# Kernel optimization log

Measured on AMD Instinct MI355X. Metric: run time of the kernel, lower is better.

## Reference

```python
import jax, jax.numpy as jnp
import numpy as np

INPUT_SIZE = 64
STATE_SIZE = 1984
OUTPUT_SIZE = 64
WIDTH = INPUT_SIZE + STATE_SIZE  # 2048
ID_PROP = 0.9
SEQ_LEN = 128
BATCH = 128


def setup_inputs() -> dict:
    key = jax.random.key(0)
    k1, k2, k3 = jax.random.split(key, 3)
    # xavier-uniform bound for square [WIDTH, WIDTH] linears
    bound = float(np.sqrt(6.0 / (WIDTH + WIDTH)))
    W1 = jax.random.uniform(k1, (WIDTH, WIDTH), jnp.float32, -bound, bound)
    W2 = jax.random.uniform(k2, (WIDTH, WIDTH), jnp.float32, -bound, bound)
    b1 = jnp.zeros((WIDTH,), jnp.float32)
    b2 = jnp.zeros((WIDTH,), jnp.float32)
    inp = jax.random.normal(k3, (SEQ_LEN, BATCH, INPUT_SIZE), jnp.float32)
    return {"input": inp, "W1": W1, "b1": b1, "W2": W2, "b2": b2}


def reference(input, W1, b1, W2, b2):
    T, B, _ = input.shape
    # initial output_stream is zeros of width WIDTH, broadcast over batch
    state0 = jnp.zeros((B, WIDTH), input.dtype)

    def step(state, x_t):
        # Shift: concat(input, state) then keep first WIDTH elems
        s = jnp.concatenate([x_t, state[:, :STATE_SIZE]], axis=-1)  # [B, WIDTH]
        # Res: r*p + (1-p) * fc2(|fc1(s)|)
        h = jnp.abs(s @ W1.T + b1)
        s = s * ID_PROP + (1.0 - ID_PROP) * (h @ W2.T + b2)
        return s, None

    state, _ = jax.lax.scan(step, state0, input)
    return state[..., -OUTPUT_SIZE:]
```

## Files before the change

### kernel.cpp

```cpp
#include <hip/hip_runtime.h>
#include <stdint.h>


#define NSTEPS 128
#define NB 128
#define WID 2048
#define SS 1984

typedef __attribute__((ext_vector_type(8))) short short8;
typedef __attribute__((ext_vector_type(4))) short short4v;
typedef __attribute__((ext_vector_type(4))) float f32x4;
typedef unsigned long long u64;

static __device__ __forceinline__ short f2bf(float f) {
  union { float f; unsigned u; } v; v.f = f;
  unsigned r = (v.u + 0x7fffu + ((v.u >> 16) & 1u)) >> 16;
  return (short)r;
}

static __device__ __forceinline__ short8 pack8(f32x4 lo, f32x4 hi) {
  short8 r;
  r[0] = f2bf(lo[0]); r[1] = f2bf(lo[1]); r[2] = f2bf(lo[2]); r[3] = f2bf(lo[3]);
  r[4] = f2bf(hi[0]); r[5] = f2bf(hi[1]); r[6] = f2bf(hi[2]); r[7] = f2bf(hi[3]);
  return r;
}

static __device__ __forceinline__ void ast64(void* p, u64 v) {
  __hip_atomic_store((u64*)p, v, __ATOMIC_RELAXED, __HIP_MEMORY_SCOPE_AGENT);
}
static __device__ __forceinline__ unsigned ald32(const unsigned* p) {
  return __hip_atomic_load(p, __ATOMIC_RELAXED, __HIP_MEMORY_SCOPE_AGENT);
}

#define LLCLD(d, a) \
  asm volatile("global_load_dwordx4 %0, %1, off sc1" : "=&v"(d) : "v"(a))
#define VMW(n) do { \
    asm volatile("s_waitcnt vmcnt(" #n ")" ::: "memory"); \
    __builtin_amdgcn_sched_barrier(0); \
  } while (0)

#define P1ISSUE(b, X) do {                                                    \
    if (kb == 0 && (b) == 0) {   \
      const float* q0_ = inp + ((size_t)t * NB + m0) * 64 + q8;               \
      const float* q1_ = inp + ((size_t)t * NB + m1) * 64 + q8;               \
      X[0] = pack8(*(const f32x4*)q0_, *(const f32x4*)(q0_ + 4));             \
      X[1] = pack8(*(const f32x4*)q1_, *(const f32x4*)(q1_ + 4));             \
      X[2] = pack8(*(const f32x4*)(q0_ + 32), *(const f32x4*)(q0_ + 36));     \
      X[3] = pack8(*(const f32x4*)(q1_ + 32), *(const f32x4*)(q1_ + 36));     \
      const short* s_ = SbOld + (size_t)slabL * 1024;                         \
      LLCLD(X[4], (s_ + rowoff0));           LLCLD(X[5], (s_ + rowoff1));     \
      LLCLD(X[6], (s_ + 4096 + rowoff0));    LLCLD(X[7], (s_ + 4096 + rowoff1)); \
    } else {                                                                  \
      const short* s_ = SbOld + (size_t)(kb / 8 + 16 * (b) - 8 + slabL) * 1024; \
      LLCLD(X[0], (s_ + rowoff0));           LLCLD(X[1], (s_ + rowoff1));     \
      LLCLD(X[2], (s_ + 4096 + rowoff0));    LLCLD(X[3], (s_ + 4096 + rowoff1)); \
      LLCLD(X[4], (s_ + 8192 + rowoff0));    LLCLD(X[5], (s_ + 8192 + rowoff1)); \
      LLCLD(X[6], (s_ + 12288 + rowoff0));   LLCLD(X[7], (s_ + 12288 + rowoff1)); \
    }                                                                         \
  } while (0)

#define P1MFMA(b, X) do {                                                     \
    a00 = __builtin_amdgcn_mfma_f32_16x16x32_bf16(X[0], B1[4*(b)+0][0], a00, 0,0,0); \
    a01 = __builtin_amdgcn_mfma_f32_16x16x32_bf16(X[0], B1[4*(b)+0][1], a01, 0,0,0); \
    a10 = __builtin_amdgcn_mfma_f32_16x16x32_bf16(X[1], B1[4*(b)+0][0], a10, 0,0,0); \
    a11 = __builtin_amdgcn_mfma_f32_16x16x32_bf16(X[1], B1[4*(b)+0][1], a11, 0,0,0); \
    a00 = __builtin_amdgcn_mfma_f32_16x16x32_bf16(X[2], B1[4*(b)+1][0], a00, 0,0,0); \
    a01 = __builtin_amdgcn_mfma_f32_16x16x32_bf16(X[2], B1[4*(b)+1][1], a01, 0,0,0); \
    a10 = __builtin_amdgcn_mfma_f32_16x16x32_bf16(X[3], B1[4*(b)+1][0], a10, 0,0,0); \
    a11 = __builtin_amdgcn_mfma_f32_16x16x32_bf16(X[3], B1[4*(b)+1][1], a11, 0,0,0); \
    a00 = __builtin_amdgcn_mfma_f32_16x16x32_bf16(X[4], B1[4*(b)+2][0], a00, 0,0,0); \
    a01 = __builtin_amdgcn_mfma_f32_16x16x32_bf16(X[4], B1[4*(b)+2][1], a01, 0,0,0); \
    a10 = __builtin_amdgcn_mfma_f32_16x16x32_bf16(X[5], B1[4*(b)+2][0], a10, 0,0,0); \
    a11 = __builtin_amdgcn_mfma_f32_16x16x32_bf16(X[5], B1[4*(b)+2][1], a11, 0,0,0); \
    a00 = __builtin_amdgcn_mfma_f32_16x16x32_bf16(X[6], B1[4*(b)+3][0], a00, 0,0,0); \
    a01 = __builtin_amdgcn_mfma_f32_16x16x32_bf16(X[6], B1[4*(b)+3][1], a01, 0,0,0); \
    a10 = __builtin_amdgcn_mfma_f32_16x16x32_bf16(X[7], B1[4*(b)+3][0], a10, 0,0,0); \
    a11 = __builtin_amdgcn_mfma_f32_16x16x32_bf16(X[7], B1[4*(b)+3][1], a11, 0,0,0); \
  } while (0)

#define P2ISSUE(b, X) do {                                                    \
    const short* h_ = hb + (size_t)(kb / 8 + 16 * (b) + slabL) * 1024;        \
    LLCLD(X[0], (h_ + rowoff0));           LLCLD(X[1], (h_ + rowoff1));       \
    LLCLD(X[2], (h_ + 4096 + rowoff0));    LLCLD(X[3], (h_ + 4096 + rowoff1)); \
    LLCLD(X[4], (h_ + 8192 + rowoff0));    LLCLD(X[5], (h_ + 8192 + rowoff1)); \
    LLCLD(X[6], (h_ + 12288 + rowoff0));   LLCLD(X[7], (h_ + 12288 + rowoff1)); \
  } while (0)

#define P2MFMA(b, X) do {                                                     \
    c00 = __builtin_amdgcn_mfma_f32_16x16x32_bf16(X[0], B2[4*(b)+0][0], c00, 0,0,0); \
    c01 = __builtin_amdgcn_mfma_f32_16x16x32_bf16(X[0], B2[4*(b)+0][1], c01, 0,0,0); \
    c10 = __builtin_amdgcn_mfma_f32_16x16x32_bf16(X[1], B2[4*(b)+0][0], c10, 0,0,0); \
    c11 = __builtin_amdgcn_mfma_f32_16x16x32_bf16(X[1], B2[4*(b)+0][1], c11, 0,0,0); \
    c00 = __builtin_amdgcn_mfma_f32_16x16x32_bf16(X[2], B2[4*(b)+1][0], c00, 0,0,0); \
    c01 = __builtin_amdgcn_mfma_f32_16x16x32_bf16(X[2], B2[4*(b)+1][1], c01, 0,0,0); \
    c10 = __builtin_amdgcn_mfma_f32_16x16x32_bf16(X[3], B2[4*(b)+1][0], c10, 0,0,0); \
    c11 = __builtin_amdgcn_mfma_f32_16x16x32_bf16(X[3], B2[4*(b)+1][1], c11, 0,0,0); \
    c00 = __builtin_amdgcn_mfma_f32_16x16x32_bf16(X[4], B2[4*(b)+2][0], c00, 0,0,0); \
    c01 = __builtin_amdgcn_mfma_f32_16x16x32_bf16(X[4], B2[4*(b)+2][1], c01, 0,0,0); \
    c10 = __builtin_amdgcn_mfma_f32_16x16x32_bf16(X[5], B2[4*(b)+2][0], c10, 0,0,0); \
    c11 = __builtin_amdgcn_mfma_f32_16x16x32_bf16(X[5], B2[4*(b)+2][1], c11, 0,0,0); \
    c00 = __builtin_amdgcn_mfma_f32_16x16x32_bf16(X[6], B2[4*(b)+3][0], c00, 0,0,0); \
    c01 = __builtin_amdgcn_mfma_f32_16x16x32_bf16(X[6], B2[4*(b)+3][1], c01, 0,0,0); \
    c10 = __builtin_amdgcn_mfma_f32_16x16x32_bf16(X[7], B2[4*(b)+3][0], c10, 0,0,0); \
    c11 = __builtin_amdgcn_mfma_f32_16x16x32_bf16(X[7], B2[4*(b)+3][1], c11, 0,0,0); \
  } while (0)

__global__ __launch_bounds__(256, 1)
void resrnn_kernel(const float* __restrict__ inp, const float* __restrict__ W1,
                   const float* __restrict__ b1f, const float* __restrict__ W2,
                   const float* __restrict__ b2f, float* __restrict__ out,
                   unsigned char* __restrict__ ws)
{
  const int tid   = threadIdx.x;
  const int bid   = blockIdx.x;
  const int group = bid & 3;
  const int chunk = bid >> 2;
  const int mbase = group * 32;
  const int n0    = chunk * 32;
  const int wave  = tid >> 6;
  const int lane  = tid & 63;
  const int l15   = lane & 15;
  const int q8    = (lane >> 4) * 8;
  const int kb    = wave * 512;
  const int slabL = lane >> 4;

  unsigned* sgen = (unsigned*)(ws + group * 8192);
  unsigned* hgen = (unsigned*)(ws + group * 8192 + 4096);
  float* Sf0 = (float*)(ws + 32768);
  float* Sf1 = (float*)(ws + 32768 + 1015808);
  short* Sb0 = (short*)(ws + 32768 + 2031616);
  short* Sb1 = (short*)(ws + 32768 + 2539520);
  short* hb  = (short*)(ws + 32768 + 3047424);

  __shared__ float red[4][16][65];

  short8 B1[16][2], B2[16][2];
#pragma unroll
  for (int ks = 0; ks < 16; ++ks) {
#pragma unroll
    for (int nt = 0; nt < 2; ++nt) {
      const float* p1 = W1 + (size_t)(n0 + nt * 16 + l15) * WID + (kb + ks * 32 + q8);
      B1[ks][nt] = pack8(*(const f32x4*)p1, *(const f32x4*)(p1 + 4));
      const float* p2 = W2 + (size_t)(n0 + nt * 16 + l15) * WID + (kb + ks * 32 + q8);
      B2[ks][nt] = pack8(*(const f32x4*)p2, *(const f32x4*)(p2 + 4));
    }
  }

  const int m0 = mbase + l15;
  const int m1 = mbase + 16 + l15;
  const int rowoff0 = (mbase + l15) * 8;
  const int rowoff1 = rowoff0 + 128;

  const int ml   = (tid & 63) >> 1;
  const int nl   = ((tid >> 6) << 3) + ((tid & 1) << 2);
  const int mrow = mbase + ml;
  const int c0   = n0 + nl;
  const size_t toff = (size_t)(n0 / 8 + wave) * 1024 + (size_t)mrow * 8
                    + (size_t)((tid & 1) << 2);

  const f32x4 b1r = *(const f32x4*)(b1f + c0);
  const f32x4 b2r = *(const f32x4*)(b2f + c0);

  const int p1pc = 16 * wave + l15 - 2;
  const bool p1needA = (lane < 16) && (p1pc >= 0);
  const bool p1needB = (lane == 16) && (chunk >= 2);
  const unsigned* p1fp =
      p1needA ? (sgen + p1pc * 16)
              : (sgen + (chunk >= 2 ? chunk - 2 : 0) * 16);
  const unsigned* p2fp = hgen + (16 * wave + l15) * 16;

  short8 xa[8], xb[8], xc[8], xd[8];

#pragma unroll 1
  for (int t = 0; t < NSTEPS; ++t) {
    const float* SfOld = (t & 1) ? Sf1 : Sf0;
    float*       SfNew = (t & 1) ? Sf0 : Sf1;
    const short* SbOld = (t & 1) ? Sb1 : Sb0;
    short*       SbNew = (t & 1) ? Sb0 : Sb1;

    f32x4 a00{}, a01{}, a10{}, a11{};
    f32x4 prevv;
    if (t == 0) {
      prevv = (c0 < 64) ? *(const f32x4*)(inp + (size_t)mrow * 64 + c0)
                        : f32x4{0.f, 0.f, 0.f, 0.f};
      if (kb == 0) {
        const float* q0_ = inp + (size_t)m0 * 64 + q8;
        const float* q1_ = inp + (size_t)m1 * 64 + q8;
        short8 x0 = pack8(*(const f32x4*)q0_, *(const f32x4*)(q0_ + 4));
        short8 x1 = pack8(*(const f32x4*)q1_, *(const f32x4*)(q1_ + 4));
        short8 x2 = pack8(*(const f32x4*)(q0_ + 32), *(const f32x4*)(q0_ + 36));
        short8 x3 = pack8(*(const f32x4*)(q1_ + 32), *(const f32x4*)(q1_ + 36));
        a00 = __builtin_amdgcn_mfma_f32_16x16x32_bf16(x0, B1[0][0], a00, 0, 0, 0);
        a01 = __builtin_amdgcn_mfma_f32_16x16x32_bf16(x0, B1[0][1], a01, 0, 0, 0);
        a10 = __builtin_amdgcn_mfma_f32_16x16x32_bf16(x1, B1[0][0], a10, 0, 0, 0);
        a11 = __builtin_amdgcn_mfma_f32_16x16x32_bf16(x1, B1[0][1], a11, 0, 0, 0);
        a00 = __builtin_amdgcn_mfma_f32_16x16x32_bf16(x2, B1[1][0], a00, 0, 0, 0);
        a01 = __builtin_amdgcn_mfma_f32_16x16x32_bf16(x2, B1[1][1], a01, 0, 0, 0);
        a10 = __builtin_amdgcn_mfma_f32_16x16x32_bf16(x3, B1[1][0], a10, 0, 0, 0);
        a11 = __builtin_amdgcn_mfma_f32_16x16x32_bf16(x3, B1[1][1], a11, 0, 0, 0);
      }
    } else {
      {
        const unsigned tgt = (unsigned)t;
        bool pend = p1needA || p1needB;
        for (;;) {
          if (pend && ald32(p1fp) >= tgt) pend = false;
          if (__ballot(pend) == 0ull) break;
        }
      }
      if (chunk < 2) {
        prevv = *(const f32x4*)(inp + ((size_t)t * NB + mrow) * 64 + c0);
        P1ISSUE(0, xa); P1ISSUE(1, xb); P1ISSUE(2, xc); P1ISSUE(3, xd);
        VMW(24); P1MFMA(0, xa);
        VMW(16); P1MFMA(1, xb);
        VMW(8);  P1MFMA(2, xc);
        VMW(0);  P1MFMA(3, xd);
      } else {
        P1ISSUE(0, xa); P1ISSUE(1, xb); P1ISSUE(2, xc); P1ISSUE(3, xd);
        LLCLD(prevv, (SfOld + toff - 8192));
        VMW(25); P1MFMA(0, xa);
        VMW(17); P1MFMA(1, xb);
        VMW(9);  P1MFMA(2, xc);
        VMW(1);  P1MFMA(3, xd);
      }
    }
#pragma unroll
    for (int r = 0; r < 4; ++r) {
      red[wave][r][lane]      = a00[r];
      red[wave][4 + r][lane]  = a01[r];
      red[wave][8 + r][lane]  = a10[r];
      red[wave][12 + r][lane] = a11[r];
    }
    __syncthreads();
    {
      short4v hv;
#pragma unroll
      for (int j = 0; j < 4; ++j) {
        const int nn   = nl + j;
        const int lidx = ((ml >> 2) & 3) * 16 + (nn & 15);
        const int ridx = (ml >> 4) * 8 + (nn >> 4) * 4 + (ml & 3);
        float s = red[0][ridx][lidx] + red[1][ridx][lidx]
                + red[2][ridx][lidx] + red[3][ridx][lidx];
        s += b1r[j];
        hv[j] = f2bf(fabsf(s));
      }
      union { short4v s; u64 u; } hu; hu.s = hv;
      ast64(hb + toff, hu.u);
    }
    __syncthreads();
    if (tid == 0)
      __hip_atomic_store(hgen + chunk * 16, (unsigned)t + 1,
                         __ATOMIC_RELAXED, __HIP_MEMORY_SCOPE_AGENT);

    f32x4 c00{}, c01{}, c10{}, c11{};
    {
      {
        const unsigned tgt = (unsigned)t + 1;
        bool pend = (lane < 16);
        for (;;) {
          if (pend && ald32(p2fp) >= tgt) pend = false;
          if (__ballot(pend) == 0ull) break;
        }
      }
      P2ISSUE(0, xa); P2ISSUE(1, xb); P2ISSUE(2, xc); P2ISSUE(3, xd);
      VMW(24); P2MFMA(0, xa);
      VMW(16); P2MFMA(1, xb);
      VMW(8);  P2MFMA(2, xc);
      VMW(0);  P2MFMA(3, xd);
    }
#pragma unroll
    for (int r = 0; r < 4; ++r) {
      red[wave][r][lane]      = c00[r];
      red[wave][4 + r][lane]  = c01[r];
      red[wave][8 + r][lane]  = c10[r];
      red[wave][12 + r][lane] = c11[r];
    }
    __syncthreads();
    if (t < NSTEPS - 1) {
      if (n0 < SS) {
        f32x4 gv;
#pragma unroll
        for (int j = 0; j < 4; ++j) {
          const int nn   = nl + j;
          const int lidx = ((ml >> 2) & 3) * 16 + (nn & 15);
          const int ridx = (ml >> 4) * 8 + (nn >> 4) * 4 + (ml & 3);
          gv[j] = red[0][ridx][lidx] + red[1][ridx][lidx]
                + red[2][ridx][lidx] + red[3][ridx][lidx] + b2r[j];
        }
        f32x4 sv; short4v sb;
#pragma unroll
        for (int j = 0; j < 4; ++j) {
          float vv = 0.9f * prevv[j] + 0.1f * gv[j];
          sv[j] = vv; sb[j] = f2bf(vv);
        }
        union { f32x4 f; u64 u[2]; } sfu; sfu.f = sv;
        float* pf = SfNew + toff;
        ast64(pf, sfu.u[0]);
        ast64(pf + 2, sfu.u[1]);
        union { short4v s; u64 u; } sbu; sbu.s = sb;
        ast64(SbNew + toff, sbu.u);
      }
      __syncthreads();
      if (tid == 0 && chunk < 62)
        __hip_atomic_store(sgen + chunk * 16, (unsigned)t + 1,
                           __ATOMIC_RELAXED, __HIP_MEMORY_SCOPE_AGENT);
    } else {
      if (n0 >= SS) {
        f32x4 gv;
#pragma unroll
        for (int j = 0; j < 4; ++j) {
          const int nn   = nl + j;
          const int lidx = ((ml >> 2) & 3) * 16 + (nn & 15);
          const int ridx = (ml >> 4) * 8 + (nn >> 4) * 4 + (ml & 3);
          gv[j] = red[0][ridx][lidx] + red[1][ridx][lidx]
                + red[2][ridx][lidx] + red[3][ridx][lidx] + b2r[j];
        }
        f32x4 ov;
#pragma unroll
        for (int j = 0; j < 4; ++j) ov[j] = 0.9f * prevv[j] + 0.1f * gv[j];
        *(f32x4*)(out + (size_t)mrow * 64 + (c0 - SS)) = ov;
      }
    }
  }
}

extern "C" void kernel_launch(void* const* d_in, const int* in_sizes, int n_in,
                              void* d_out, int out_size, void* d_ws, size_t ws_size,
                              hipStream_t stream)
{
  (void)in_sizes; (void)n_in; (void)out_size; (void)ws_size;
  const float* inp = (const float*)d_in[0];
  const float* W1  = (const float*)d_in[1];
  const float* b1  = (const float*)d_in[2];
  const float* W2  = (const float*)d_in[3];
  const float* b2  = (const float*)d_in[4];
  float* out = (float*)d_out;

  hipMemsetAsync(d_ws, 0, 32768, stream);
  resrnn_kernel<<<dim3(256), dim3(256), 0, stream>>>(
      inp, W1, b1, W2, b2, out, (unsigned char*)d_ws);
}
```

Measured before the change: 1.078 ms.

## Read same-XCD producer data through a cached mirror instead of LLC-coherent loads

After: 1.376 ms. 1.28x slower.

```diff
diff --git a/kernel.cpp b/kernel.cpp
--- a/kernel.cpp
+++ b/kernel.cpp
@@ -37,6 +37,16 @@
 #define VMW(n) do { \
     asm volatile("s_waitcnt vmcnt(" #n ")" ::: "memory"); \
     __builtin_amdgcn_sched_barrier(0); \
+  } while (0)
+
+#define CLD(d, gaddr, maddr, bit, msk) do {                                   \
+    if ((msk) & (1u << (bit))) {                                              \
+      asm volatile("global_load_dwordx4 %0, %1, off sc0"                      \
+                   : "=&v"(d) : "v"(maddr));                                  \
+    } else {                                                                  \
+      asm volatile("global_load_dwordx4 %0, %1, off sc1"                      \
+                   : "=&v"(d) : "v"(gaddr));                                  \
+    }                                                                         \
   } while (0)
 
 #define P1ISSUE(b, X) do {                                                    \
@@ -47,15 +57,23 @@
       X[1] = pack8(*(const f32x4*)q1_, *(const f32x4*)(q1_ + 4));             \
       X[2] = pack8(*(const f32x4*)(q0_ + 32), *(const f32x4*)(q0_ + 36));     \
       X[3] = pack8(*(const f32x4*)(q1_ + 32), *(const f32x4*)(q1_ + 36));     \
-      const short* s_ = SbOld + (size_t)slabL * 1024;                         \
-      LLCLD(X[4], (s_ + rowoff0));           LLCLD(X[5], (s_ + rowoff1));     \
-      LLCLD(X[6], (s_ + 4096 + rowoff0));    LLCLD(X[7], (s_ + 4096 + rowoff1)); \
+      const short* g_ = SbOld  + (size_t)slabL * 1024;                        \
+      const short* l_ = SbMOld + (size_t)slabL * 1024;                        \
+      CLD(X[4], (g_ + rowoff0),        (l_ + rowoff0),        2, m1s);        \
+      CLD(X[5], (g_ + rowoff1),        (l_ + rowoff1),        2, m1s);        \
+      CLD(X[6], (g_ + 4096 + rowoff0), (l_ + 4096 + rowoff0), 3, m1s);        \
+      CLD(X[7], (g_ + 4096 + rowoff1), (l_ + 4096 + rowoff1), 3, m1s);        \
     } else {                                                                  \
-      const short* s_ = SbOld + (size_t)(kb / 8 + 16 * (b) - 8 + slabL) * 1024; \
-      LLCLD(X[0], (s_ + rowoff0));           LLCLD(X[1], (s_ + rowoff1));     \
-      LLCLD(X[2], (s_ + 4096 + rowoff0));    LLCLD(X[3], (s_ + 4096 + rowoff1)); \
-      LLCLD(X[4], (s_ + 8192 + rowoff0));    LLCLD(X[5], (s_ + 8192 + rowoff1)); \
-      LLCLD(X[6], (s_ + 12288 + rowoff0));   LLCLD(X[7], (s_ + 12288 + rowoff1)); \
+      const size_t sb_ = (size_t)(kb / 8 + 16 * (b) - 8 + slabL) * 1024;      \
+      const short* g_ = SbOld + sb_;  const short* l_ = SbMOld + sb_;         \
+      CLD(X[0], (g_ + rowoff0),         (l_ + rowoff0),         4*(b)+0, m1s);\
+      CLD(X[1], (g_ + rowoff1),         (l_ + rowoff1),         4*(b)+0, m1s);\
+      CLD(X[2], (g_ + 4096 + rowoff0),  (l_ + 4096 + rowoff0),  4*(b)+1, m1s);\
+      CLD(X[3], (g_ + 4096 + rowoff1),  (l_ + 4096 + rowoff1),  4*(b)+1, m1s);\
+      CLD(X[4], (g_ + 8192 + rowoff0),  (l_ + 8192 + rowoff0),  4*(b)+2, m1s);\
+      CLD(X[5], (g_ + 8192 + rowoff1),  (l_ + 8192 + rowoff1),  4*(b)+2, m1s);\
+      CLD(X[6], (g_ + 12288 + rowoff0), (l_ + 12288 + rowoff0), 4*(b)+3, m1s);\
+      CLD(X[7], (g_ + 12288 + rowoff1), (l_ + 12288 + rowoff1), 4*(b)+3, m1s);\
     }                                                                         \
   } while (0)
 
@@ -79,11 +97,16 @@
   } while (0)
 
 #define P2ISSUE(b, X) do {                                                    \
-    const short* h_ = hb + (size_t)(kb / 8 + 16 * (b) + slabL) * 1024;        \
-    LLCLD(X[0], (h_ + rowoff0));           LLCLD(X[1], (h_ + rowoff1));       \
-    LLCLD(X[2], (h_ + 4096 + rowoff0));    LLCLD(X[3], (h_ + 4096 + rowoff1)); \
-    LLCLD(X[4], (h_ + 8192 + rowoff0));    LLCLD(X[5], (h_ + 8192 + rowoff1)); \
-    LLCLD(X[6], (h_ + 12288 + rowoff0));   LLCLD(X[7], (h_ + 12288 + rowoff1)); \
+    const size_t hb_ = (size_t)(kb / 8 + 16 * (b) + slabL) * 1024;            \
+    const short* g_ = hb + hb_;  const short* l_ = hbM + hb_;                 \
+    CLD(X[0], (g_ + rowoff0),         (l_ + rowoff0),         4*(b)+0, m2s);  \
+    CLD(X[1], (g_ + rowoff1),         (l_ + rowoff1),         4*(b)+0, m2s);  \
+    CLD(X[2], (g_ + 4096 + rowoff0),  (l_ + 4096 + rowoff0),  4*(b)+1, m2s);  \
+    CLD(X[3], (g_ + 4096 + rowoff1),  (l_ + 4096 + rowoff1),  4*(b)+1, m2s);  \
+    CLD(X[4], (g_ + 8192 + rowoff0),  (l_ + 8192 + rowoff0),  4*(b)+2, m2s);  \
+    CLD(X[5], (g_ + 8192 + rowoff1),  (l_ + 8192 + rowoff1),  4*(b)+2, m2s);  \
+    CLD(X[6], (g_ + 12288 + rowoff0), (l_ + 12288 + rowoff0), 4*(b)+3, m2s);  \
+    CLD(X[7], (g_ + 12288 + rowoff1), (l_ + 12288 + rowoff1), 4*(b)+3, m2s);  \
   } while (0)
 
 #define P2MFMA(b, X) do {                                                     \
@@ -126,13 +149,38 @@
 
   unsigned* sgen = (unsigned*)(ws + group * 8192);
   unsigned* hgen = (unsigned*)(ws + group * 8192 + 4096);
-  float* Sf0 = (float*)(ws + 32768);
-  float* Sf1 = (float*)(ws + 32768 + 1015808);
-  short* Sb0 = (short*)(ws + 32768 + 2031616);
-  short* Sb1 = (short*)(ws + 32768 + 2539520);
-  short* hb  = (short*)(ws + 32768 + 3047424);
+  unsigned* xtab = (unsigned*)(ws + 32768);
+  unsigned* verd = (unsigned*)(ws + 33792);
+  float* Sf0  = (float*)(ws + 36864);
+  float* Sf1  = (float*)(ws + 36864 + 1015808);
+  short* Sb0  = (short*)(ws + 36864 + 2031616);
+  short* Sb1  = (short*)(ws + 36864 + 2539520);
+  short* hb   = (short*)(ws + 36864 + 3047424);
+  short* hbM  = (short*)(ws + 36864 + 3571712);
+  short* SbM0 = (short*)(ws + 36864 + 4096000);
+  short* SbM1 = (short*)(ws + 36864 + 4603904);
 
   __shared__ float red[4][16][65];
+  __shared__ unsigned hcnt[10];
+
+  unsigned xraw;
+  asm("s_getreg_b32 %0, hwreg(HW_REG_XCC_ID)" : "=s"(xraw));
+  const unsigned myx = xraw + 1u;
+  if (tid == 0)
+    __hip_atomic_store(xtab + bid, myx, __ATOMIC_RELAXED, __HIP_MEMORY_SCOPE_AGENT);
+  if (bid == 0) {
+    unsigned v;
+    for (;;) { v = ald32(xtab + tid); if (v) break; __builtin_amdgcn_s_sleep(2); }
+    if (tid < 10) hcnt[tid] = 0;
+    __syncthreads();
+    atomicAdd(&hcnt[v <= 8 ? v : 0], 1u);
+    __syncthreads();
+    if (tid == 0) {
+      bool ok = (hcnt[0] == 0);
+      for (int q = 1; q <= 8; ++q) if (hcnt[q] != 32) ok = false;
+      __hip_atomic_store(verd, ok ? 1u : 2u, __ATOMIC_RELAXED, __HIP_MEMORY_SCOPE_AGENT);
+    }
+  }
 
   short8 B1[16][2], B2[16][2];
 #pragma unroll
@@ -145,6 +193,20 @@
       B2[ks][nt] = pack8(*(const f32x4*)p2, *(const f32x4*)(p2 + 4));
     }
   }
+
+  unsigned vd;
+  for (;;) { vd = ald32(verd); if (vd) break; __builtin_amdgcn_s_sleep(2); }
+  unsigned m1v = 0, m2v = 0;
+  if (vd == 1) {
+    for (int j = 0; j < 16; ++j) {
+      const int p2c = 16 * wave + j;
+      if (ald32(xtab + ((p2c << 2) | group)) == myx) m2v |= 1u << j;
+      const int p1c = p2c - 2;
+      if (p1c >= 0 && ald32(xtab + ((p1c << 2) | group)) == myx) m1v |= 1u << j;
+    }
+  }
+  const unsigned m1s = __builtin_amdgcn_readfirstlane(m1v);
+  const unsigned m2s = __builtin_amdgcn_readfirstlane(m2v);
 
   const int m0 = mbase + l15;
   const int m1 = mbase + 16 + l15;
@@ -173,10 +235,12 @@
 
 #pragma unroll 1
   for (int t = 0; t < NSTEPS; ++t) {
-    const float* SfOld = (t & 1) ? Sf1 : Sf0;
-    float*       SfNew = (t & 1) ? Sf0 : Sf1;
-    const short* SbOld = (t & 1) ? Sb1 : Sb0;
-    short*       SbNew = (t & 1) ? Sb0 : Sb1;
+    const float* SfOld  = (t & 1) ? Sf1 : Sf0;
+    float*       SfNew  = (t & 1) ? Sf0 : Sf1;
+    const short* SbOld  = (t & 1) ? Sb1 : Sb0;
+    short*       SbNew  = (t & 1) ? Sb0 : Sb1;
+    const short* SbMOld = (t & 1) ? SbM1 : SbM0;
+    short*       SbMNew = (t & 1) ? SbM0 : SbM1;
 
     f32x4 a00{}, a01{}, a10{}, a11{};
     f32x4 prevv;
@@ -246,6 +310,7 @@
       }
       union { short4v s; u64 u; } hu; hu.s = hv;
       ast64(hb + toff, hu.u);
+      *(u64*)(hbM + toff) = hu.u;
     }
     __syncthreads();
     if (tid == 0)
@@ -299,6 +364,7 @@
         ast64(pf + 2, sfu.u[1]);
         union { short4v s; u64 u; } sbu; sbu.s = sb;
         ast64(SbNew + toff, sbu.u);
+        *(u64*)(SbMNew + toff) = sbu.u;
       }
       __syncthreads();
       if (tid == 0 && chunk < 62)
@@ -336,7 +402,7 @@
   const float* b2  = (const float*)d_in[4];
   float* out = (float*)d_out;
 
-  hipMemsetAsync(d_ws, 0, 32768, stream);
+  hipMemsetAsync(d_ws, 0, 34048, stream);
   resrnn_kernel<<<dim3(256), dim3(256), 0, stream>>>(
       inp, W1, b1, W2, b2, out, (unsigned char*)d_ws);
 }
```
